# Optimization experiments

Hardware: AMD Instinct MI355X
Metric: run time of the kernel (lower is better)

## Reference

```python
import jax, jax.numpy as jnp
import numpy as np

N_NODES = 100000
N_EDGES = 1600000
D_IN = 100      # entity/relation embedding dim (rel_weight is [100,50])
D_HID = 50      # conv1 out_channels (hard-coded in ctor)
N_REL = 237     # relation_num; rel_embedding doubled -> 474 relation types
N_REL2 = 2 * N_REL
N_BASES = 5     # num_bases hard-coded
N_CLASS = 50    # class_num


def setup_inputs() -> dict:
    key = jax.random.key(0)
    ks = jax.random.split(key, 12)
    x = jax.random.normal(ks[0], (N_NODES, D_IN), dtype=jnp.float32)
    edge_index = jax.random.randint(ks[1], (2, N_EDGES), 0, N_NODES)
    edge_type = jax.random.randint(ks[2], (N_EDGES,), 0, N_REL2)
    rel_embedding = jax.random.normal(ks[3], (N_REL, D_IN), dtype=jnp.float32) * 0.1
    rel_weight = jax.random.uniform(ks[4], (D_IN, D_HID), dtype=jnp.float32)  # nn.Parameter(torch.rand)
    basis1 = jax.random.normal(ks[5], (N_BASES, D_IN, D_HID), dtype=jnp.float32) * 0.1
    comp1 = jax.random.normal(ks[6], (N_REL2, N_BASES), dtype=jnp.float32) * 0.1
    root1 = jax.random.normal(ks[7], (D_IN, D_HID), dtype=jnp.float32) * 0.1
    bias1 = jnp.zeros((D_HID,), dtype=jnp.float32)
    basis2 = jax.random.normal(ks[8], (N_BASES, D_HID, N_CLASS), dtype=jnp.float32) * 0.1
    comp2 = jax.random.normal(ks[9], (N_REL2, N_BASES), dtype=jnp.float32) * 0.1
    root2 = jax.random.normal(ks[10], (D_HID, N_CLASS), dtype=jnp.float32) * 0.1
    bias2 = jnp.zeros((N_CLASS,), dtype=jnp.float32)
    return {
        "x": x, "edge_index": edge_index, "edge_type": edge_type, "target_node": 5,
        "rel_embedding": rel_embedding, "rel_weight": rel_weight,
        "basis1": basis1, "comp1": comp1, "root1": root1, "bias1": bias1,
        "basis2": basis2, "comp2": comp2, "root2": root2, "bias2": bias2,
    }


def _transe_conv(x, src, dst, e_emb, comp_e, basis, root_w, bias):
    """RGCN-style conv with TransE compose and basis decomposition.
    x: [N, Fin], e_emb: [E, Fin], comp_e: [E, B], basis: [B, Fin, Fout].
    message m = x[src] + e_emb; out_e = m @ (sum_b comp_e[b] * basis[b]); mean-agg at dst.
    """
    m = x[src] + e_emb  # [E, Fin] -- dominant gather
    acc = jnp.zeros((m.shape[0], basis.shape[2]), dtype=m.dtype)
    for b in range(basis.shape[0]):  # small fixed basis count (5)
        acc = acc + comp_e[:, b:b + 1] * (m @ basis[b])
    agg = jax.ops.segment_sum(acc, dst, num_segments=x.shape[0])  # [N, Fout]
    cnt = jax.ops.segment_sum(jnp.ones((dst.shape[0],), dtype=x.dtype), dst,
                              num_segments=x.shape[0])
    mean = agg / jnp.maximum(cnt, 1.0)[:, None]
    return mean + x @ root_w + bias


def reference(x, edge_index, edge_type, target_node, rel_embedding, rel_weight,
              basis1, comp1, root1, bias1, basis2, comp2, root2, bias2):
    # x[target_node] = 0
    x = x.at[target_node].set(0.0)
    src, dst = edge_index[0], edge_index[1]
    # rel_embedding doubled (forward + inverse relations)
    rel_full = jnp.concatenate([rel_embedding, rel_embedding], axis=0)  # [2R, D_IN]
    e1 = rel_full[edge_type]                                            # [E, D_IN]
    h = _transe_conv(x, src, dst, e1, comp1[edge_type], basis1, root1, bias1)
    rel2 = rel_full @ rel_weight                                        # [2R, D_HID]
    e2 = rel2[edge_type]                                                # [E, D_HID]
    h = _transe_conv(h, src, dst, e2, comp2[edge_type], basis2, root2, bias2)
    return jax.nn.log_softmax(h, axis=1)
```

## Files before the change

kernel.cpp:

```cpp
#include <hip/hip_runtime.h>
#include <hip/hip_bf16.h>

typedef __hip_bfloat16 bf16;

#define N_NODES 100000
#define N_EDGES 1600000
#define D_IN    100
#define D_HID   50
#define N_REL   237
#define N_REL2  474
#define N_CLASS 50

#define NBUCK    196
#define BSHIFT   9
#define BCAP     10240
#define BIN_EPB  1024
#define BIN_BLKS ((N_EDGES + BIN_EPB - 1) / BIN_EPB)

#define MID_PACK1_BLKS 160
#define MID_PACK2_BLKS 80
#define MID_REL_BLKS   474
#define MID_TOTAL (BIN_BLKS + MID_PACK1_BLKS + MID_PACK2_BLKS + MID_REL_BLKS)

#define GEMM_BLKS ((N_NODES + 63) / 64)

#define RED_BLKS (N_NODES / 8)

typedef __attribute__((ext_vector_type(8))) short short8;
typedef __attribute__((ext_vector_type(4))) float f32x4;
typedef __attribute__((ext_vector_type(2))) float f32x2;

__device__ __forceinline__ float b2f(bf16 v) { return __bfloat162float(v); }
__device__ __forceinline__ bf16  f2b(float v) { return __float2bfloat16(v); }

__device__ __forceinline__ float ldw(const void* p, int idx, int isbf) {
    return isbf ? b2f(((const bf16*)p)[idx]) : ((const float*)p)[idx];
}

#if __has_builtin(__builtin_amdgcn_cvt_f32_fp8) && __has_builtin(__builtin_amdgcn_cvt_pk_fp8_f32)
#define F8_HW 1
#endif
#if __has_builtin(__builtin_amdgcn_cvt_pk_f32_fp8)
#define F8PK_HW 1
#endif

__device__ __forceinline__ float f8tof(unsigned u) {
#ifdef F8_HW
    return __builtin_amdgcn_cvt_f32_fp8((int)u, 0);
#else
    unsigned s = u >> 7, e = (u >> 3) & 0xF, m = u & 7;
    float v;
    if (e == 0) v = (float)m * 0.001953125f;
    else        v = (float)(8 + m) * __builtin_ldexpf(1.f, (int)e - 10);
    return s ? -v : v;
#endif
}

#ifdef F8_HW
#define F8SEL(u, s) __builtin_amdgcn_cvt_f32_fp8((int)(u), (s))
#else
#define F8SEL(u, s) f8tof(((u) >> (8 * (s))) & 0xFFu)
#endif

template <bool HI>
__device__ __forceinline__ f32x2 f8pk(unsigned u) {
#ifdef F8PK_HW
    return __builtin_amdgcn_cvt_pk_f32_fp8((int)u, HI);
#else
    f32x2 r;
    r.x = F8SEL(u, HI ? 2 : 0);
    r.y = F8SEL(u, HI ? 3 : 1);
    return r;
#endif
}

__device__ __forceinline__ unsigned f8enc_sw(float v) {
    unsigned bits = __float_as_uint(v);
    unsigned s = bits >> 31;
    float a = fabsf(v);
    if (a < 0.0009765625f) return s << 7;
    if (a >= 448.f) return (s << 7) | 0x7E;
    int E = (int)((bits >> 23) & 0xFF) - 127;
    unsigned m = bits & 0x7FFFFF;
    if (E < -6) {
        int q = (int)rintf(a * 512.f);
        if (q > 7) q = 7;
        return (s << 7) | (unsigned)q;
    }
    unsigned lsb = (m >> 20) & 1, rnd = (m >> 19) & 1;
    unsigned sticky = (m & 0x7FFFF) ? 1u : 0u;
    unsigned m3 = (m >> 20) + (rnd & (sticky | lsb));
    if (m3 == 8) { m3 = 0; E += 1; }
    if (E > 8) return (s << 7) | 0x7E;
    return (s << 7) | ((unsigned)(E + 7) << 3) | m3;
}

__device__ __forceinline__ unsigned pk4_f8(float v0, float v1, float v2, float v3) {
#ifdef F8_HW
    int p = __builtin_amdgcn_cvt_pk_fp8_f32(v0, v1, 0, false);
    p = __builtin_amdgcn_cvt_pk_fp8_f32(v2, v3, p, true);
    return (unsigned)p;
#else
    return f8enc_sw(v0) | (f8enc_sw(v1) << 8) | (f8enc_sw(v2) << 16) | (f8enc_sw(v3) << 24);
#endif
}

__global__ void k_detect(const unsigned short* __restrict__ xr, int* __restrict__ flag) {
    int tid = threadIdx.x;
    int cnt = 0;
    for (int i = tid; i < 4096; i += 256) {
        unsigned short u = xr[2 * i];
        unsigned e = (u >> 7) & 0xFF;
        bool pl = (e >= 107 && e <= 132) || ((u & 0x7FFF) == 0);
        cnt += pl ? 1 : 0;
    }
    __shared__ int sh[256];
    sh[tid] = cnt;
    __syncthreads();
    for (int s = 128; s > 0; s >>= 1) {
        if (tid < s) sh[tid] += sh[tid + s];
        __syncthreads();
    }
    if (tid == 0) flag[0] = (sh[0] >= 3072) ? 1 : 0;
}

__device__ __forceinline__ void job_bin(int blk, const int* __restrict__ src,
                                        const int* __restrict__ dst,
                                        const int* __restrict__ et,
                                        unsigned* __restrict__ bucketFill,
                                        unsigned long long* __restrict__ staging) {
    __shared__ unsigned lhist[NBUCK];
    __shared__ unsigned lstart[NBUCK];
    __shared__ unsigned gbase[NBUCK];
    __shared__ unsigned scan_tmp[NBUCK];
    __shared__ unsigned long long lval[BIN_EPB];
    __shared__ unsigned ltgt[BIN_EPB];
    int tid = threadIdx.x;
    int base = blk * BIN_EPB;
    int n = N_EDGES - base; if (n > BIN_EPB) n = BIN_EPB;

    for (int i = tid; i < NBUCK; i += 256) lhist[i] = 0;
    __syncthreads();

    unsigned bb[4], rr[4];
    unsigned long long vv[4];
#pragma unroll
    for (int j = 0; j < 4; ++j) {
        int i = j * 256 + tid;
        bb[j] = 0xFFFFFFFFu;
        if (i < n) {
            int e = base + i;
            unsigned d = (unsigned)dst[e];
            unsigned b = d >> BSHIFT;
            bb[j] = b;
            rr[j] = atomicAdd(&lhist[b], 1u);
            vv[j] = ((unsigned long long)d << 32) |
                    (unsigned long long)((unsigned)src[e] | ((unsigned)et[e] << 17));
        }
    }
    __syncthreads();
    unsigned v0 = (tid < NBUCK) ? lhist[tid] : 0;
    if (tid < NBUCK) scan_tmp[tid] = v0;
    __syncthreads();
    for (int s = 1; s < NBUCK; s <<= 1) {
        unsigned t = 0;
        if (tid < NBUCK && tid >= (unsigned)s) t = scan_tmp[tid - s];
        __syncthreads();
        if (tid < NBUCK) scan_tmp[tid] += t;
        __syncthreads();
    }
    if (tid < NBUCK) {
        lstart[tid] = scan_tmp[tid] - v0;
        gbase[tid] = (v0 > 0) ? atomicAdd(&bucketFill[tid], v0) : 0u;
    }
    __syncthreads();
#pragma unroll
    for (int j = 0; j < 4; ++j) {
        if (bb[j] != 0xFFFFFFFFu) {
            unsigned pos = lstart[bb[j]] + rr[j];
            unsigned off = gbase[bb[j]] + rr[j];
            lval[pos] = vv[j];
            ltgt[pos] = (off < BCAP) ? (bb[j] * BCAP + off) : 0xFFFFFFFFu;
        }
    }
    __syncthreads();
    for (int i = tid; i < n; i += 256) {
        unsigned t = ltgt[i];
        if (t != 0xFFFFFFFFu) staging[t] = lval[i];
    }
}

__device__ __forceinline__ void job_pack(int blk, const void* basis, const void* root,
                                         bf16* Wb, int KL, int isbf) {
    int g = blk * 256 + threadIdx.x;
    int ks = g / 10240;
    int r = g - ks * 10240;
    int ct = r >> 9;
    int r2 = r & 511;
    int l = r2 >> 3, j = r2 & 7;
    int k = ks * 32 + ((l >> 4) << 3) + j;
    int n = ct * 16 + (l & 15);
    float v = 0.f;
    if (k < KL && n < 300) {
        if (n < 250) { int b = n / 50, f = n - b * 50; v = ldw(basis, (b * KL + k) * 50 + f, isbf); }
        else         v = ldw(root, k * 50 + (n - 250), isbf);
    }
    Wb[g] = f2b(v);
}

template<int ISBF>
__device__ __forceinline__ void job_rel(int t,
        const void* __restrict__ rel_emb, const void* __restrict__ rel_w,
        const void* __restrict__ basis1, const void* __restrict__ comp1,
        const void* __restrict__ basis2, const void* __restrict__ comp2,
        float* __restrict__ rt1, float* __restrict__ rt2,
        float* __restrict__ c81, float* __restrict__ c82) {
    int tid = threadIdx.x;
    __shared__ float rf[D_IN];
    __shared__ float r2s[D_HID];
    int tm = (t >= N_REL) ? t - N_REL : t;
    if (tid < D_IN) rf[tid] = ldw(rel_emb, tm * D_IN + tid, ISBF);
    if (tid < 8) {
        c81[t * 8 + tid] = (tid < 5) ? ldw(comp1, t * 5 + tid, ISBF) : 0.f;
        c82[t * 8 + tid] = (tid < 5) ? ldw(comp2, t * 5 + tid, ISBF) : 0.f;
    }
    __syncthreads();
    if (tid < 50) {
        int f = tid;
        float a = 0.f;
        for (int b = 0; b < 5; ++b) {
            float cb = ldw(comp1, t * 5 + b, ISBF);
            float s = 0.f;
            for (int k = 0; k < D_IN; ++k) s += rf[k] * ldw(basis1, (b * D_IN + k) * 50 + f, ISBF);
            a += cb * s;
        }
        rt1[t * 50 + f] = a;
        float s2 = 0.f;
        for (int k = 0; k < D_IN; ++k) s2 += rf[k] * ldw(rel_w, k * 50 + f, ISBF);
        r2s[f] = s2;
    }
    __syncthreads();
    if (tid < 50) {
        int f = tid;
        float a = 0.f;
        for (int b = 0; b < 5; ++b) {
            float cb = ldw(comp2, t * 5 + b, ISBF);
            float s = 0.f;
            for (int k = 0; k < 50; ++k) s += r2s[k] * ldw(basis2, (b * 50 + k) * 50 + f, ISBF);
            a += cb * s;
        }
        rt2[t * 50 + f] = a;
    }
}

__global__ __launch_bounds__(256) void k_mid(const int* __restrict__ srcp,
                                             const int* __restrict__ dstp,
                                             const int* __restrict__ etp,
                                             unsigned* __restrict__ bucketFill,
                                             unsigned long long* __restrict__ staging,
                                             const int* __restrict__ flag,
                                             const void* rel_emb, const void* rel_w,
                                             const void* basis1, const void* comp1,
                                             const void* root1,
                                             const void* basis2, const void* comp2,
                                             const void* root2,
                                             bf16* __restrict__ Wb1, bf16* __restrict__ Wb2,
                                             float* __restrict__ rt1, float* __restrict__ rt2,
                                             float* __restrict__ c81, float* __restrict__ c82) {
    int blk = blockIdx.x;
    if (blk < BIN_BLKS) { job_bin(blk, srcp, dstp, etp, bucketFill, staging); return; }
    blk -= BIN_BLKS;
    int isbf = flag[0];
    if (blk < MID_PACK1_BLKS) { job_pack(blk, basis1, root1, Wb1, D_IN, isbf); return; }
    blk -= MID_PACK1_BLKS;
    if (blk < MID_PACK2_BLKS) { job_pack(blk, basis2, root2, Wb2, D_HID, isbf); return; }
    blk -= MID_PACK2_BLKS;
    if (isbf) job_rel<1>(blk, rel_emb, rel_w, basis1, comp1, basis2, comp2, rt1, rt2, c81, c82);
    else      job_rel<0>(blk, rel_emb, rel_w, basis1, comp1, basis2, comp2, rt1, rt2, c81, c82);
}

__device__ __forceinline__ void job_bucket(int b, char* shraw,
        const unsigned long long* __restrict__ staging,
        const unsigned* __restrict__ bucketFill,
        int* __restrict__ offs, unsigned* __restrict__ se) {
    unsigned* hist = (unsigned*)shraw;
    unsigned* excl = hist + 512;
    unsigned* bfs  = excl + 512;
    unsigned* tmp  = bfs + 256;
    int tid = threadIdx.x;

    if (tid < NBUCK) {
        unsigned c = bucketFill[tid];
        bfs[tid] = (c > BCAP) ? BCAP : c;
    }
    hist[tid] = 0; hist[tid + 256] = 0;
    __syncthreads();
    for (int s = 1; s < NBUCK; s <<= 1) {
        unsigned t = 0;
        if (tid < NBUCK && tid >= s) t = bfs[tid - s];
        __syncthreads();
        if (tid < NBUCK) bfs[tid] += t;
        __syncthreads();
    }
    unsigned base = (b == 0) ? 0u : bfs[b - 1];
    unsigned cnt = bfs[b] - base;

    const unsigned long long* p = staging + (size_t)b * BCAP;
    for (unsigned i = tid; i < cnt; i += 256) {
        unsigned d = (unsigned)(p[i] >> 32);
        atomicAdd(&hist[d & 511], 1u);
    }
    __syncthreads();
    unsigned h0 = hist[2 * tid], h1 = hist[2 * tid + 1];
    tmp[tid] = h0 + h1;
    __syncthreads();
    for (int s = 1; s < 256; s <<= 1) {
        unsigned t = (tid >= s) ? tmp[tid - s] : 0u;
        __syncthreads();
        tmp[tid] += t;
        __syncthreads();
    }
    unsigned pe = (tid > 0) ? tmp[tid - 1] : 0u;
    excl[2 * tid]     = pe;
    excl[2 * tid + 1] = pe + h0;
    hist[2 * tid] = 0; hist[2 * tid + 1] = 0;
    __syncthreads();

#pragma unroll
    for (int q = 0; q < 2; ++q) {
        int li = 2 * tid + q;
        int node = b * 512 + li;
        if (node < N_NODES) offs[node] = (int)(base + excl[li]);
        if (node == N_NODES - 1) offs[N_NODES] = (int)(base + cnt);
    }

    for (unsigned i = tid; i < cnt; i += 256) {
        unsigned long long v = p[i];
        unsigned ld = ((unsigned)(v >> 32)) & 511u;
        unsigned r = atomicAdd(&hist[ld], 1u);
        se[base + excl[ld] + r] = (unsigned)v;
    }
}

template<int KP, bool ZT, bool RAWX>
__global__ __launch_bounds__(256) void k_gemm_b(const void* __restrict__ Xraw,
                                                const int* __restrict__ flag,
                                                const bf16* __restrict__ Wb,
                                                unsigned char* __restrict__ Y8,
                                                bf16* __restrict__ R, int M,
                                                const int* __restrict__ tgt,
                                                const unsigned long long* __restrict__ staging,
                                                const unsigned* __restrict__ bucketFill,
                                                int* __restrict__ offs,
                                                unsigned* __restrict__ se,
                                                int nbuckBlks) {
    constexpr int AP = KP + 8;
    __shared__ __attribute__((aligned(16))) char shraw[64 * 320 * 2];
    if ((int)blockIdx.x < nbuckBlks) {
        job_bucket(blockIdx.x, shraw, staging, bucketFill, offs, se);
        return;
    }
    int gblk = blockIdx.x - nbuckBlks;
    bf16* smem = (bf16*)shraw;
    int tid = threadIdx.x;
    int w = tid >> 6, lane = tid & 63;
    int quad = lane >> 4, cIn = lane & 15;
    int base_row = gblk * 64;

    if (RAWX) {
        int isbf = flag[0];
        for (int i = tid; i < 64 * 64; i += 256) {
            int r = i >> 6, c2 = (i & 63) << 1;
            int row = base_row + r; if (row > M - 1) row = M - 1;
            unsigned pkd = 0;
            if (c2 < 100) {
                if (isbf) {
                    pkd = *(const unsigned*)((const unsigned short*)Xraw + (size_t)row * 100 + c2);
                } else {
                    const float* xp = (const float*)Xraw + (size_t)row * 100 + c2;
                    float vx = xp[0], vy = xp[1];
                    bf16 b0 = f2b(vx), b1 = f2b(vy);
                    pkd = (unsigned)*(unsigned short*)&b0 | ((unsigned)*(unsigned short*)&b1 << 16);
                }
            }
            *(unsigned*)(&smem[r * AP + c2]) = pkd;
        }
    } else {
        const bf16* X = (const bf16*)Xraw;
        const int TOT = 64 * KP / 8;
        for (int i = tid; i < TOT; i += 256) {
            int e8 = i * 8;
            int r = e8 / KP, c = e8 - r * KP;
            int row = base_row + r; if (row > M - 1) row = M - 1;
            *(uint4*)(&smem[r * AP + c]) = *(const uint4*)(&X[(size_t)row * KP + c]);
        }
    }
    __syncthreads();

    f32x4 acc[20];
#pragma unroll
    for (int i = 0; i < 20; ++i) acc[i] = (f32x4){0.f, 0.f, 0.f, 0.f};

#pragma unroll
    for (int ks = 0; ks < KP / 32; ++ks) {
        short8 a = *(const short8*)(&smem[(w * 16 + cIn) * AP + ks * 32 + quad * 8]);
#pragma unroll
        for (int ct = 0; ct < 20; ++ct) {
            short8 b = *(const short8*)(&Wb[(size_t)((ks * 20 + ct) * 64 + lane) * 8]);
            acc[ct] = __builtin_amdgcn_mfma_f32_16x16x32_bf16(a, b, acc[ct], 0, 0, 0);
        }
    }
    __syncthreads();

#pragma unroll
    for (int ct = 0; ct < 20; ++ct)
#pragma unroll
        for (int r = 0; r < 4; ++r)
            smem[(w * 16 + quad * 4 + r) * 320 + ct * 16 + cIn] = f2b(acc[ct][r]);
    __syncthreads();

    int tv = -1;
    if (ZT) tv = tgt[0];
    int valid = M - base_row; if (valid > 64) valid = 64;

    for (int i = tid; i < valid * 64; i += 256) {
        int r = i >> 6, u = i & 63;
        int row = base_row + r;
        unsigned pbits;
        if (u < 50) {
            pbits = pk4_f8(b2f(smem[r * 320 + u]),       b2f(smem[r * 320 + 50 + u]),
                           b2f(smem[r * 320 + 100 + u]), b2f(smem[r * 320 + 150 + u]));
        } else if (u < 63) {
            int fb = (u - 50) * 4;
            float v0 = (fb + 0 < 50) ? b2f(smem[r * 320 + 200 + fb + 0]) : 0.f;
            float v1 = (fb + 1 < 50) ? b2f(smem[r * 320 + 200 + fb + 1]) : 0.f;
            float v2 = (fb + 2 < 50) ? b2f(smem[r * 320 + 200 + fb + 2]) : 0.f;
            float v3 = (fb + 3 < 50) ? b2f(smem[r * 320 + 200 + fb + 3]) : 0.f;
            pbits = pk4_f8(v0, v1, v2, v3);
        } else {
            pbits = 0u;
        }
        if (ZT && row == tv) pbits = 0u;
        *(unsigned*)(Y8 + (size_t)row * 256 + u * 4) = pbits;
    }
    for (int i = tid; i < valid * 32; i += 256) {
        int r = i >> 5, cu = i & 31;
        int row = base_row + r;
        int j0 = cu * 2, j1 = j0 + 1;
        unsigned short ua = (j0 < 50) ? *(const unsigned short*)&smem[r * 320 + 250 + j0] : 0;
        unsigned short ub = (j1 < 50) ? *(const unsigned short*)&smem[r * 320 + 250 + j1] : 0;
        unsigned u = (unsigned)ua | ((unsigned)ub << 16);
        if (ZT && row == tv) u = 0u;
        *(unsigned*)((unsigned short*)R + (size_t)row * 64 + j0) = u;
    }
}

__device__ __forceinline__ void edge_body(unsigned p, int f,
        const unsigned char* __restrict__ Y8,
        const float* __restrict__ c8, const float* __restrict__ rt,
        f32x2& acc2, float& accS) {
    unsigned ps = (unsigned)__builtin_amdgcn_readfirstlane((int)p);
    int s_ = (int)(ps & 0x1FFFFu);
    int t_ = (int)(ps >> 17);
    const unsigned char* yr = Y8 + (size_t)s_ * 256;
    unsigned a4 = *(const unsigned*)(yr + 4 * f);
    float y4 = f8tof(yr[200 + f]);
    const float* cp = c8 + t_ * 8;
    f32x4 c03 = *(const f32x4*)cp;
    float c4 = cp[4];
    float rv = rt[t_ * 50 + f];
    f32x2 y01 = f8pk<false>(a4);
    f32x2 y23 = f8pk<true>(a4);
    f32x2 cA; cA.x = c03.x; cA.y = c03.y;
    f32x2 cB; cB.x = c03.z; cB.y = c03.w;
    acc2 += cA * y01;
    acc2 += cB * y23;
    accS += rv + c4 * y4;
}

__device__ __forceinline__ void pair_reduce(const int* __restrict__ off,
        const unsigned int* __restrict__ se, const float* __restrict__ c8,
        const float* __restrict__ rt, const unsigned char* __restrict__ Y8,
        int rowA, int f, float& outA, float& outB, float& cntA, float& cntB) {
    int e0 = __builtin_amdgcn_readfirstlane(off[rowA]);
    int e1 = __builtin_amdgcn_readfirstlane(off[rowA + 1]);
    int e2 = __builtin_amdgcn_readfirstlane(off[rowA + 2]);
    f32x2 a2A; a2A.x = 0.f; a2A.y = 0.f;
    f32x2 a2B; a2B.x = 0.f; a2B.y = 0.f;
    float sA = 0.f, sB = 0.f;
    int eA = e0, eB = e1;
    while (eA + 4 <= e1 && eB + 4 <= e2) {
        unsigned pA0 = se[eA],     pA1 = se[eA + 1], pA2 = se[eA + 2], pA3 = se[eA + 3];
        unsigned pB0 = se[eB],     pB1 = se[eB + 1], pB2 = se[eB + 2], pB3 = se[eB + 3];
        edge_body(pA0, f, Y8, c8, rt, a2A, sA);
        edge_body(pB0, f, Y8, c8, rt, a2B, sB);
        edge_body(pA1, f, Y8, c8, rt, a2A, sA);
        edge_body(pB1, f, Y8, c8, rt, a2B, sB);
        edge_body(pA2, f, Y8, c8, rt, a2A, sA);
        edge_body(pB2, f, Y8, c8, rt, a2B, sB);
        edge_body(pA3, f, Y8, c8, rt, a2A, sA);
        edge_body(pB3, f, Y8, c8, rt, a2B, sB);
        eA += 4; eB += 4;
    }
    while (eA + 4 <= e1) {
        unsigned p0 = se[eA], p1 = se[eA + 1], p2 = se[eA + 2], p3 = se[eA + 3];
        edge_body(p0, f, Y8, c8, rt, a2A, sA);
        edge_body(p1, f, Y8, c8, rt, a2A, sA);
        edge_body(p2, f, Y8, c8, rt, a2A, sA);
        edge_body(p3, f, Y8, c8, rt, a2A, sA);
        eA += 4;
    }
    while (eB + 4 <= e2) {
        unsigned p0 = se[eB], p1 = se[eB + 1], p2 = se[eB + 2], p3 = se[eB + 3];
        edge_body(p0, f, Y8, c8, rt, a2B, sB);
        edge_body(p1, f, Y8, c8, rt, a2B, sB);
        edge_body(p2, f, Y8, c8, rt, a2B, sB);
        edge_body(p3, f, Y8, c8, rt, a2B, sB);
        eB += 4;
    }
    for (; eA < e1; ++eA) edge_body(se[eA], f, Y8, c8, rt, a2A, sA);
    for (; eB < e2; ++eB) edge_body(se[eB], f, Y8, c8, rt, a2B, sB);
    outA = a2A.x + a2A.y + sA;
    outB = a2B.x + a2B.y + sB;
    float nA = (float)(e1 - e0); cntA = nA > 1.f ? nA : 1.f;
    float nB = (float)(e2 - e1); cntB = nB > 1.f ? nB : 1.f;
}

__global__ __launch_bounds__(256) void k_reduce1(const int* __restrict__ off,
                                                 const unsigned int* __restrict__ se,
                                                 const float* __restrict__ c8,
                                                 const float* __restrict__ rt,
                                                 const unsigned char* __restrict__ Y8,
                                                 const bf16* __restrict__ R,
                                                 const void* __restrict__ bias_raw,
                                                 const int* __restrict__ flag,
                                                 bf16* __restrict__ h) {
    int wid = threadIdx.x >> 6, lane = threadIdx.x & 63;
    int rowA = __builtin_amdgcn_readfirstlane(blockIdx.x * 8 + wid * 2);
    int f = (lane < 50) ? lane : 49;
    float accA, accB, cntA, cntB;
    pair_reduce(off, se, c8, rt, Y8, rowA, f, accA, accB, cntA, cntB);
    float bv = ldw(bias_raw, f, flag[0]);
    float vA = accA / cntA + b2f(R[(size_t)rowA * 64 + f]) + bv;
    float vB = accB / cntB + b2f(R[(size_t)(rowA + 1) * 64 + f]) + bv;
    h[(size_t)rowA * 64 + lane]       = f2b(lane < 50 ? vA : 0.f);
    h[(size_t)(rowA + 1) * 64 + lane] = f2b(lane < 50 ? vB : 0.f);
}

__device__ __forceinline__ void softmax_store(float acc, float cnt, int row, int f,
        int lane, const bf16* __restrict__ R, float bv,
        int isbf, void* __restrict__ out) {
    float v = -INFINITY;
    if (lane < 50)
        v = acc / cnt + b2f(R[(size_t)row * 64 + f]) + bv;
    float m = v;
    for (int o = 32; o > 0; o >>= 1) m = fmaxf(m, __shfl_xor(m, o));
    float ex = (lane < 50) ? expf(v - m) : 0.f;
    float s = ex;
    for (int o = 32; o > 0; o >>= 1) s += __shfl_xor(s, o);
    float res = v - m - logf(s);
    if (lane < 50) {
        if (isbf) ((bf16*)out)[row * 50 + f] = f2b(res);
        else      ((float*)out)[row * 50 + f] = res;
    }
}

__global__ __launch_bounds__(256) void k_reduce2(const int* __restrict__ off,
                                                 const unsigned int* __restrict__ se,
                                                 const float* __restrict__ c8,
                                                 const float* __restrict__ rt,
                                                 const unsigned char* __restrict__ Y8,
                                                 const bf16* __restrict__ R,
                                                 const void* __restrict__ bias_raw,
                                                 const int* __restrict__ flag,
                                                 void* __restrict__ out) {
    int wid = threadIdx.x >> 6, lane = threadIdx.x & 63;
    int rowA = __builtin_amdgcn_readfirstlane(blockIdx.x * 8 + wid * 2);
    int f = (lane < 50) ? lane : 49;
    float accA, accB, cntA, cntB;
    pair_reduce(off, se, c8, rt, Y8, rowA, f, accA, accB, cntA, cntB);
    int isbf = flag[0];
    float bv = ldw(bias_raw, f, isbf);
    softmax_store(accA, cntA, rowA, f, lane, R, bv, isbf, out);
    softmax_store(accB, cntB, rowA + 1, f, lane, R, bv, isbf, out);
}

extern "C" void kernel_launch(void* const* d_in, const int* in_sizes, int n_in,
                              void* d_out, int out_size, void* d_ws, size_t ws_size,
                              hipStream_t stream) {
    const void* x_raw = d_in[0];
    const int*  ei    = (const int*)d_in[1];
    const int*  et    = (const int*)d_in[2];
    const int*  tgt   = (const int*)d_in[3];
    const void* rel_emb = d_in[4];
    const void* rel_w   = d_in[5];
    const void* basis1  = d_in[6];
    const void* comp1   = d_in[7];
    const void* root1   = d_in[8];
    const void* bias1   = d_in[9];
    const void* basis2  = d_in[10];
    const void* comp2   = d_in[11];
    const void* root2   = d_in[12];
    const void* bias2   = d_in[13];

    char* wsp = (char*)d_ws;
    size_t off_b = 0;
    auto alloc = [&](size_t bytes) {
        void* p = wsp + off_b;
        off_b = (off_b + bytes + 255) & ~(size_t)255;
        return p;
    };
    unsigned char* Y8 = (unsigned char*)alloc((size_t)N_NODES * 256);
    bf16*  R    = (bf16*) alloc((size_t)N_NODES * 64 * sizeof(bf16));
    bf16*  h    = (bf16*) alloc((size_t)N_NODES * 64 * sizeof(bf16));
    unsigned int* se = (unsigned int*)alloc((size_t)N_EDGES * sizeof(unsigned int));
    unsigned long long* staging = (unsigned long long*)alloc((size_t)NBUCK * BCAP * 8);
    int*   offs = (int*)  alloc((size_t)(N_NODES + 1) * sizeof(int));
    unsigned* bucketFill = (unsigned*)alloc((size_t)NBUCK * sizeof(unsigned));
    bf16*  Wb1  = (bf16*) alloc((size_t)40960 * sizeof(bf16));
    bf16*  Wb2  = (bf16*) alloc((size_t)20480 * sizeof(bf16));
    float* rt1  = (float*)alloc((size_t)N_REL2 * 50 * sizeof(float));
    float* rt2  = (float*)alloc((size_t)N_REL2 * 50 * sizeof(float));
    float* c81  = (float*)alloc((size_t)N_REL2 * 8 * sizeof(float));
    float* c82  = (float*)alloc((size_t)N_REL2 * 8 * sizeof(float));
    int*   flag = (int*)  alloc(sizeof(int));

    const int* srcp = ei;
    const int* dstp = ei + N_EDGES;

    hipMemsetAsync(bucketFill, 0, (size_t)NBUCK * sizeof(unsigned), stream);

    k_detect<<<1, 256, 0, stream>>>((const unsigned short*)x_raw, flag);

    k_mid<<<MID_TOTAL, 256, 0, stream>>>(srcp, dstp, et, bucketFill, staging, flag,
                                         rel_emb, rel_w, basis1, comp1, root1,
                                         basis2, comp2, root2,
                                         Wb1, Wb2, rt1, rt2, c81, c82);

    k_gemm_b<128, true, true><<<GEMM_BLKS + NBUCK, 256, 0, stream>>>(
        x_raw, flag, Wb1, Y8, R, N_NODES, tgt, staging, bucketFill, offs, se, NBUCK);

    k_reduce1<<<RED_BLKS, 256, 0, stream>>>(offs, se, c81, rt1, Y8, R, bias1, flag, h);

    k_gemm_b<64, false, false><<<GEMM_BLKS, 256, 0, stream>>>(
        h, flag, Wb2, Y8, R, N_NODES, nullptr, staging, bucketFill, offs, se, 0);

    k_reduce2<<<RED_BLKS, 256, 0, stream>>>(offs, se, c82, rt2, Y8, R, bias2, flag, d_out);
}
```

Baseline: 397.8 us.

## Halve GEMM row tile and split columns across waves for occupancy

The node GEMM block now covers 32 rows instead of 64. The four waves split as 2 row-groups by 2 column-halves, so each wave holds 10 accumulator tiles instead of 20. The A and C tiles get separate shared-memory regions, which removes one barrier, and the C stride is padded to 324 to reduce bank conflicts. The 4-blocks-per-SM launch bound aims to raise occupancy and latency hiding, at the cost of twice as many blocks and twice as many weight fetches per output row.

```diff
diff --git a/kernel.cpp b/kernel.cpp
--- a/kernel.cpp
+++ b/kernel.cpp
@@ -22,7 +22,9 @@
 #define MID_REL_BLKS   474
 #define MID_TOTAL (BIN_BLKS + MID_PACK1_BLKS + MID_PACK2_BLKS + MID_REL_BLKS)
 
-#define GEMM_BLKS ((N_NODES + 63) / 64)
+#define GEMM_BLKS ((N_NODES + 31) / 32)
+
+#define CST 324
 
 #define RED_BLKS (N_NODES / 8)
 
@@ -343,7 +345,7 @@
 }
 
 template<int KP, bool ZT, bool RAWX>
-__global__ __launch_bounds__(256) void k_gemm_b(const void* __restrict__ Xraw,
+__global__ __launch_bounds__(256, 4) void k_gemm_b(const void* __restrict__ Xraw,
                                                 const int* __restrict__ flag,
                                                 const bf16* __restrict__ Wb,
                                                 unsigned char* __restrict__ Y8,
@@ -355,21 +357,25 @@
                                                 unsigned* __restrict__ se,
                                                 int nbuckBlks) {
     constexpr int AP = KP + 8;
-    __shared__ __attribute__((aligned(16))) char shraw[64 * 320 * 2];
+    constexpr int CBYTES = 32 * CST * 2;
+    constexpr int ABYTES = 32 * AP * 2;
+    __shared__ __attribute__((aligned(16))) char shraw[CBYTES + ABYTES];
     if ((int)blockIdx.x < nbuckBlks) {
         job_bucket(blockIdx.x, shraw, staging, bucketFill, offs, se);
         return;
     }
     int gblk = blockIdx.x - nbuckBlks;
-    bf16* smem = (bf16*)shraw;
+    bf16* smemC = (bf16*)shraw;
+    bf16* smemA = (bf16*)(shraw + CBYTES);
     int tid = threadIdx.x;
     int w = tid >> 6, lane = tid & 63;
     int quad = lane >> 4, cIn = lane & 15;
-    int base_row = gblk * 64;
+    int rw = w & 1, cw = w >> 1;
+    int base_row = gblk * 32;
 
     if (RAWX) {
         int isbf = flag[0];
-        for (int i = tid; i < 64 * 64; i += 256) {
+        for (int i = tid; i < 32 * 64; i += 256) {
             int r = i >> 6, c2 = (i & 63) << 1;
             int row = base_row + r; if (row > M - 1) row = M - 1;
             unsigned pkd = 0;
@@ -383,59 +389,58 @@
                     pkd = (unsigned)*(unsigned short*)&b0 | ((unsigned)*(unsigned short*)&b1 << 16);
                 }
             }
-            *(unsigned*)(&smem[r * AP + c2]) = pkd;
+            *(unsigned*)(&smemA[r * AP + c2]) = pkd;
         }
     } else {
         const bf16* X = (const bf16*)Xraw;
-        const int TOT = 64 * KP / 8;
+        const int TOT = 32 * KP / 8;
         for (int i = tid; i < TOT; i += 256) {
             int e8 = i * 8;
             int r = e8 / KP, c = e8 - r * KP;
             int row = base_row + r; if (row > M - 1) row = M - 1;
-            *(uint4*)(&smem[r * AP + c]) = *(const uint4*)(&X[(size_t)row * KP + c]);
-        }
-    }
-    __syncthreads();
-
-    f32x4 acc[20];
-#pragma unroll
-    for (int i = 0; i < 20; ++i) acc[i] = (f32x4){0.f, 0.f, 0.f, 0.f};
+            *(uint4*)(&smemA[r * AP + c]) = *(const uint4*)(&X[(size_t)row * KP + c]);
+        }
+    }
+    __syncthreads();
+
+    f32x4 acc[10];
+#pragma unroll
+    for (int i = 0; i < 10; ++i) acc[i] = (f32x4){0.f, 0.f, 0.f, 0.f};
 
 #pragma unroll
     for (int ks = 0; ks < KP / 32; ++ks) {
-        short8 a = *(const short8*)(&smem[(w * 16 + cIn) * AP + ks * 32 + quad * 8]);
-#pragma unroll
-        for (int ct = 0; ct < 20; ++ct) {
-            short8 b = *(const short8*)(&Wb[(size_t)((ks * 20 + ct) * 64 + lane) * 8]);
+        short8 a = *(const short8*)(&smemA[(rw * 16 + cIn) * AP + ks * 32 + quad * 8]);
+#pragma unroll
+        for (int ct = 0; ct < 10; ++ct) {
+            short8 b = *(const short8*)(&Wb[(size_t)((ks * 20 + cw * 10 + ct) * 64 + lane) * 8]);
             acc[ct] = __builtin_amdgcn_mfma_f32_16x16x32_bf16(a, b, acc[ct], 0, 0, 0);
         }
     }
-    __syncthreads();
-
-#pragma unroll
-    for (int ct = 0; ct < 20; ++ct)
+
+#pragma unroll
+    for (int ct = 0; ct < 10; ++ct)
 #pragma unroll
         for (int r = 0; r < 4; ++r)
-            smem[(w * 16 + quad * 4 + r) * 320 + ct * 16 + cIn] = f2b(acc[ct][r]);
+            smemC[(rw * 16 + quad * 4 + r) * CST + (cw * 10 + ct) * 16 + cIn] = f2b(acc[ct][r]);
     __syncthreads();
 
     int tv = -1;
     if (ZT) tv = tgt[0];
-    int valid = M - base_row; if (valid > 64) valid = 64;
+    int valid = M - base_row; if (valid > 32) valid = 32;
 
     for (int i = tid; i < valid * 64; i += 256) {
         int r = i >> 6, u = i & 63;
         int row = base_row + r;
         unsigned pbits;
         if (u < 50) {
-            pbits = pk4_f8(b2f(smem[r * 320 + u]),       b2f(smem[r * 320 + 50 + u]),
-                           b2f(smem[r * 320 + 100 + u]), b2f(smem[r * 320 + 150 + u]));
+            pbits = pk4_f8(b2f(smemC[r * CST + u]),       b2f(smemC[r * CST + 50 + u]),
+                           b2f(smemC[r * CST + 100 + u]), b2f(smemC[r * CST + 150 + u]));
         } else if (u < 63) {
             int fb = (u - 50) * 4;
-            float v0 = (fb + 0 < 50) ? b2f(smem[r * 320 + 200 + fb + 0]) : 0.f;
-            float v1 = (fb + 1 < 50) ? b2f(smem[r * 320 + 200 + fb + 1]) : 0.f;
-            float v2 = (fb + 2 < 50) ? b2f(smem[r * 320 + 200 + fb + 2]) : 0.f;
-            float v3 = (fb + 3 < 50) ? b2f(smem[r * 320 + 200 + fb + 3]) : 0.f;
+            float v0 = (fb + 0 < 50) ? b2f(smemC[r * CST + 200 + fb + 0]) : 0.f;
+            float v1 = (fb + 1 < 50) ? b2f(smemC[r * CST + 200 + fb + 1]) : 0.f;
+            float v2 = (fb + 2 < 50) ? b2f(smemC[r * CST + 200 + fb + 2]) : 0.f;
+            float v3 = (fb + 3 < 50) ? b2f(smemC[r * CST + 200 + fb + 3]) : 0.f;
             pbits = pk4_f8(v0, v1, v2, v3);
         } else {
             pbits = 0u;
@@ -447,8 +452,8 @@
         int r = i >> 5, cu = i & 31;
         int row = base_row + r;
         int j0 = cu * 2, j1 = j0 + 1;
-        unsigned short ua = (j0 < 50) ? *(const unsigned short*)&smem[r * 320 + 250 + j0] : 0;
-        unsigned short ub = (j1 < 50) ? *(const unsigned short*)&smem[r * 320 + 250 + j1] : 0;
+        unsigned short ua = (j0 < 50) ? *(const unsigned short*)&smemC[r * CST + 250 + j0] : 0;
+        unsigned short ub = (j1 < 50) ? *(const unsigned short*)&smemC[r * CST + 250 + j1] : 0;
         unsigned u = (unsigned)ua | ((unsigned)ub << 16);
         if (ZT && row == tv) u = 0u;
         *(unsigned*)((unsigned short*)R + (size_t)row * 64 + j0) = u;
```

Result: faster. 360.9 us (-9.3%).
